# Optimization experiments

Measured on AMD Instinct MI355X. Metric: run time of the kernel, lower is better.

## Reference

```python
import jax, jax.numpy as jnp
import numpy as np

N_NODES = 10000
N_EDGES = 320000
IN_DIM = 512
HID = 64
H0 = 8
OUT = 64
H1 = 1
NEG_SLOPE = 0.2


def gat_layer(h, src, dst, W, attn_l, attn_r, n_nodes, activation=None):
    # h: (N, F_in); W: (F_in, H*D); attn_l/attn_r: (H, D)
    H, D = attn_l.shape
    feat = (h @ W).reshape(n_nodes, H, D)            # (N, H, D)
    el = jnp.einsum('nhd,hd->nh', feat, attn_l)      # (N, H)
    er = jnp.einsum('nhd,hd->nh', feat, attn_r)      # (N, H)
    e = jax.nn.leaky_relu(el[src] + er[dst], NEG_SLOPE)  # (E, H)
    # edge softmax over incoming edges of each destination node
    m = jax.ops.segment_max(e, dst, num_segments=n_nodes)   # (N, H), -inf for isolated
    m = jnp.where(jnp.isfinite(m), m, 0.0)
    ex = jnp.exp(e - m[dst])                         # (E, H)
    s = jax.ops.segment_sum(ex, dst, num_segments=n_nodes)  # (N, H)
    alpha = ex / s[dst]                              # (E, H)
    # weighted aggregation: out[dst] += alpha * feat[src]
    out = jax.ops.segment_sum(alpha[:, :, None] * feat[src], dst,
                              num_segments=n_nodes)  # (N, H, D)
    if activation is not None:
        out = activation(out)
    return out


def setup_inputs() -> dict:
    key = jax.random.key(0)
    ks = jax.random.split(key, 9)
    h = jax.random.normal(ks[0], (N_NODES, IN_DIM), dtype=jnp.float32)
    src = jax.random.randint(ks[1], (N_EDGES,), 0, N_NODES, dtype=jnp.int32)
    dst = jax.random.randint(ks[2], (N_EDGES,), 0, N_NODES, dtype=jnp.int32)
    W1 = jax.random.normal(ks[3], (IN_DIM, H0 * HID), dtype=jnp.float32) / np.sqrt(IN_DIM)
    attn_l1 = jax.random.normal(ks[4], (H0, HID), dtype=jnp.float32) / np.sqrt(HID)
    attn_r1 = jax.random.normal(ks[5], (H0, HID), dtype=jnp.float32) / np.sqrt(HID)
    W2 = jax.random.normal(ks[6], (H0 * HID, H1 * OUT), dtype=jnp.float32) / np.sqrt(H0 * HID)
    attn_l2 = jax.random.normal(ks[7], (H1, OUT), dtype=jnp.float32) / np.sqrt(OUT)
    attn_r2 = jax.random.normal(ks[8], (H1, OUT), dtype=jnp.float32) / np.sqrt(OUT)
    return {"h": h, "src": src, "dst": dst, "W1": W1, "attn_l1": attn_l1,
            "attn_r1": attn_r1, "W2": W2, "attn_l2": attn_l2, "attn_r2": attn_r2}


def reference(h, src, dst, W1, attn_l1, attn_r1, W2, attn_l2, attn_r2):
    # layer 1: elu activation, concat heads (flatten)
    x = gat_layer(h, src, dst, W1, attn_l1, attn_r1, N_NODES, activation=jax.nn.elu)
    x = x.reshape(N_NODES, H0 * HID)
    # layer 2: no activation, mean over heads
    x = gat_layer(x, src, dst, W2, attn_l2, attn_r2, N_NODES, activation=None)
    return x.mean(axis=1)  # (N, OUT)
```

## Files before the change

kernel.cpp:

```cpp
#include <hip/hip_runtime.h>
#include <hip/hip_bf16.h>
#include <math.h>

typedef unsigned int u32;
typedef unsigned short ushort;

constexpr int N_NODES = 10000;
constexpr int N_EDGES = 320000;
constexpr float NEG_SLOPE = 0.2f;

typedef __attribute__((ext_vector_type(8))) _Float16 half8;
typedef __attribute__((ext_vector_type(4))) float f32x4;
typedef __attribute__((ext_vector_type(16))) float f32x16;

__device__ __forceinline__ float lrelu(float x) { return x > 0.f ? x : NEG_SLOPE * x; }
__device__ __forceinline__ float elu(float x)   { return x > 0.f ? x : (expf(x) - 1.f); }

__device__ __forceinline__ ushort f2h(float x) {
    _Float16 h = (_Float16)x;
    return __builtin_bit_cast(ushort, h);
}
__device__ __forceinline__ float h2f(ushort u) {
    return (float)__builtin_bit_cast(_Float16, u);
}

__device__ __forceinline__ void gload16(const void* g, void* l) {
    __builtin_amdgcn_global_load_lds(
        (__attribute__((address_space(1))) void*)g,
        (__attribute__((address_space(3))) void*)l, 16, 0, 0);
}

constexpr int NB_HIST  = (N_EDGES + 255) / 256;
constexpr int NB_T1    = 64;
constexpr int NB_T2    = 8;
constexpr int NB_WLR2  = 2;
constexpr int NB_PRE   = NB_HIST + NB_T1 + NB_T2 + NB_WLR2;
constexpr int NB_SPLIT = (N_NODES * 512 / 4) / 256;

__global__ void prep1_kernel(const float4* __restrict__ h4,
                             ushort* __restrict__ xh,
                             const int* __restrict__ dst, int* __restrict__ counts,
                             int* __restrict__ rank,
                             const float* __restrict__ W1, ushort* __restrict__ w1t,
                             const float* __restrict__ W2, ushort* __restrict__ w2t,
                             const float* __restrict__ al2, const float* __restrict__ ar2,
                             float* __restrict__ wl2, float* __restrict__ wr2) {
    __shared__ float smem[64][65];
    const int b = blockIdx.x;
    if (b < NB_HIST) {
        const int i = b * 256 + threadIdx.x;
        if (i < N_EDGES) rank[i] = atomicAdd(&counts[dst[i]], 1);
    } else if (b < NB_HIST + NB_T1 + NB_T2) {
        const int t0 = b - NB_HIST;
        const bool isW1 = t0 < NB_T1;
        const float* W = isW1 ? W1 : W2;
        ushort* wt = isW1 ? w1t : w2t;
        const int N  = isW1 ? 512 : 64;
        const int t  = isW1 ? t0 : (t0 - NB_T1);
        const int ti = isW1 ? (t & 7) : t;
        const int tj = isW1 ? (t >> 3) : 0;
        const int c  = threadIdx.x & 63;
        const int r0 = threadIdx.x >> 6;
#pragma unroll
        for (int p = 0; p < 16; p++) {
            const int r = p * 4 + r0;
            smem[r][c] = W[(size_t)(ti * 64 + r) * N + tj * 64 + c];
        }
        __syncthreads();
#pragma unroll
        for (int p = 0; p < 16; p++) {
            const int rr = p * 4 + r0;
            wt[(size_t)(tj * 64 + rr) * 512 + ti * 64 + c] = f2h(smem[c][rr]);
        }
    } else if (b < NB_PRE) {
        const int k = (b - NB_HIST - NB_T1 - NB_T2) * 256 + threadIdx.x;
        float sl = 0.f, sr = 0.f;
#pragma unroll 8
        for (int d = 0; d < 64; d++) {
            const float w = W2[(size_t)k * 64 + d];
            sl += w * al2[d];
            sr += w * ar2[d];
        }
        wl2[k] = sl;
        wr2[k] = sr;
    } else {
        const int i = (b - NB_PRE) * 256 + threadIdx.x;
        const float4 v = h4[i];
        *(ushort4*)&xh[i * 4] = make_ushort4(f2h(v.x), f2h(v.y), f2h(v.z), f2h(v.w));
    }
}

__global__ void prep2_scan_kernel(const int* __restrict__ counts, int* __restrict__ offs) {
    __shared__ int wsum[4];
    const int tid = threadIdx.x;
    const int lane = tid & 63, wave = tid >> 6;
    const int base = tid * 40;
    int v[40];
    int s = 0;
#pragma unroll
    for (int i = 0; i < 40; i++) {
        v[i] = (base + i < N_NODES) ? counts[base + i] : 0;
        s += v[i];
    }
    int ps = s;
#pragma unroll
    for (int o = 1; o < 64; o <<= 1) {
        const int t = __shfl_up(ps, o);
        if (lane >= o) ps += t;
    }
    if (lane == 63) wsum[wave] = ps;
    __syncthreads();
    if (tid < 4) {
        int t = wsum[tid];
#pragma unroll
        for (int o = 1; o < 4; o <<= 1) {
            const int u = __shfl_up(t, o);
            if (tid >= o) t += u;
        }
        wsum[tid] = t;
    }
    __syncthreads();
    const int wbase = (wave > 0) ? wsum[wave - 1] : 0;
    int run = wbase + ps - s;
#pragma unroll
    for (int i = 0; i < 40; i++) {
        if (base + i < N_NODES) offs[base + i + 1] = run + v[i];
        run += v[i];
    }
    if (tid == 0) offs[0] = 0;
}

constexpr int NB_GEMM1 = ((N_NODES + 63) / 64) * 4;
constexpr int NB_SCAT  = (N_EDGES + 255) / 256;

__global__ __launch_bounds__(256) void gemm1_scatter_kernel(
    const ushort* __restrict__ A, const ushort* __restrict__ B,
    ushort* __restrict__ Cout, int M,
    const float* __restrict__ attn_l, const float* __restrict__ attn_r,
    float* __restrict__ elp, float* __restrict__ erp,
    const int* __restrict__ src, const int* __restrict__ dst,
    const int* __restrict__ rank, const int* __restrict__ offs,
    int* __restrict__ srcs) {
    constexpr int BM = 64, BN = 128, BK = 64, K = 512, N = 512;

    if ((int)blockIdx.x >= NB_GEMM1) {
        const int i = ((int)blockIdx.x - NB_GEMM1) * 256 + threadIdx.x;
        if (i < N_EDGES) srcs[offs[dst[i]] + rank[i]] = src[i];
        return;
    }

    __shared__ __align__(16) ushort sA[2][BM * BK];
    __shared__ __align__(16) ushort sB[2][BN * BK];

    const int tid = threadIdx.x;
    const int wave = tid >> 6, lane = tid & 63;
    const int m0 = ((int)blockIdx.x >> 2) * BM, n0 = ((int)blockIdx.x & 3) * BN;
    const int wm = wave >> 1, wn = wave & 1;
    const int l31 = lane & 31, lh = lane >> 5;

    size_t abyte[2]; int afb[2];
#pragma unroll
    for (int p = 0; p < 2; p++) {
        const int fb = tid * 16 + p * 4096;
        const int r = fb >> 7, s = (fb >> 4) & 7;
        int ar = m0 + r; if (ar > M - 1) ar = M - 1;
        abyte[p] = (size_t)ar * (K * 2) + (size_t)((s ^ (r & 7)) << 4);
        afb[p] = fb;
    }
    size_t bbyte[4]; int bfb[4];
#pragma unroll
    for (int p = 0; p < 4; p++) {
        const int fb = tid * 16 + p * 4096;
        const int r = fb >> 7, s = (fb >> 4) & 7;
        bbyte[p] = (size_t)(n0 + r) * (K * 2) + (size_t)((s ^ (r & 7)) << 4);
        bfb[p] = fb;
    }

    f32x16 acc[2] = {};

    const int rA = wm * 32 + l31;
    const u32 aoff = rA * 128, axr = rA & 7;
    u32 boff[2], bxr[2];
#pragma unroll
    for (int ni = 0; ni < 2; ni++) {
        const int rB = wn * 64 + ni * 32 + l31;
        boff[ni] = rB * 128; bxr[ni] = rB & 7;
    }

#pragma unroll
    for (int p = 0; p < 2; p++) gload16((const char*)A + abyte[p], (char*)&sA[0][0] + afb[p]);
#pragma unroll
    for (int p = 0; p < 4; p++) gload16((const char*)B + bbyte[p], (char*)&sB[0][0] + bfb[p]);
    __syncthreads();

    int cur = 0;
    for (int k0 = 0; k0 < K; k0 += BK) {
        if (k0 + BK < K) {
            const size_t kb = (size_t)(k0 + BK) * 2;
#pragma unroll
            for (int p = 0; p < 2; p++)
                gload16((const char*)A + abyte[p] + kb, (char*)&sA[cur ^ 1][0] + afb[p]);
#pragma unroll
            for (int p = 0; p < 4; p++)
                gload16((const char*)B + bbyte[p] + kb, (char*)&sB[cur ^ 1][0] + bfb[p]);
        }
        const char* pA = (const char*)&sA[cur][0];
        const char* pB = (const char*)&sB[cur][0];
#pragma unroll
        for (int ks = 0; ks < 4; ks++) {
            const u32 sl = ks * 2 + lh;
            const half8 ah = *(const half8*)(pA + aoff + ((sl ^ axr) << 4));
#pragma unroll
            for (int ni = 0; ni < 2; ni++) {
                const half8 bh = *(const half8*)(pB + boff[ni] + ((sl ^ bxr[ni]) << 4));
                acc[ni] = __builtin_amdgcn_mfma_f32_32x32x16_f16(ah, bh, acc[ni], 0, 0, 0);
            }
        }
        __syncthreads();
        cur ^= 1;
    }

#pragma unroll
    for (int reg = 0; reg < 16; reg++) {
        const int grow = m0 + wm * 32 + (reg & 3) + 8 * (reg >> 2) + 4 * lh;
        if (grow < M) {
#pragma unroll
            for (int ni = 0; ni < 2; ni++) {
                const int gcol = n0 + wn * 64 + ni * 32 + l31;
                Cout[(size_t)grow * N + gcol] = f2h(acc[ni][reg]);
            }
        }
    }

    const int head = (n0 + wn * 64) >> 6;
    float alv[2], arv[2];
#pragma unroll
    for (int ni = 0; ni < 2; ni++) {
        alv[ni] = attn_l[head * 64 + ni * 32 + l31];
        arv[ni] = attn_r[head * 64 + ni * 32 + l31];
    }
#pragma unroll
    for (int reg = 0; reg < 16; reg++) {
        float pl = acc[0][reg] * alv[0] + acc[1][reg] * alv[1];
        float pr = acc[0][reg] * arv[0] + acc[1][reg] * arv[1];
#pragma unroll
        for (int o = 1; o < 32; o <<= 1) {
            pl += __shfl_xor(pl, o);
            pr += __shfl_xor(pr, o);
        }
        const int grow = m0 + wm * 32 + (reg & 3) + 8 * (reg >> 2) + 4 * lh;
        if (l31 == 0 && grow < M) {
            elp[grow * 8 + head] = pl;
            erp[grow * 8 + head] = pr;
        }
    }
}

__global__ __launch_bounds__(256) void gemm2_kernel(
    const ushort* __restrict__ A, const ushort* __restrict__ B,
    ushort* __restrict__ Cout, int M) {
    constexpr int BM = 32, BN = 64, BK = 64, K = 512, N = 64;

    __shared__ __align__(16) ushort sA[2][BM * BK];
    __shared__ __align__(16) ushort sB[2][BN * BK];

    const int tid = threadIdx.x;
    const int wave = tid >> 6, lane = tid & 63;
    const int m0 = blockIdx.x * BM;
    const int wm = wave >> 1, wn = wave & 1;
    const int quad = lane >> 4, l15 = lane & 15;

    const int fa = tid * 16;
    const int ra = fa >> 7, sa_ = (fa >> 4) & 7;
    int arow = m0 + ra; if (arow > M - 1) arow = M - 1;
    const size_t abyte = (size_t)arow * (K * 2) + (size_t)((sa_ ^ (ra & 7)) << 4);

    size_t bbyte[2]; int bfb[2];
#pragma unroll
    for (int p = 0; p < 2; p++) {
        const int fb = tid * 16 + p * 4096;
        const int r = fb >> 7, s = (fb >> 4) & 7;
        bbyte[p] = (size_t)r * (K * 2) + (size_t)((s ^ (r & 7)) << 4);
        bfb[p] = fb;
    }

    f32x4 acc[2] = {};
    const int rA = wm * 16 + l15;
    const u32 aoff = rA * 128, axr = rA & 7;
    u32 boff[2], bxr[2];
#pragma unroll
    for (int ni = 0; ni < 2; ni++) {
        const int rB = wn * 32 + ni * 16 + l15;
        boff[ni] = rB * 128; bxr[ni] = rB & 7;
    }

    gload16((const char*)A + abyte, (char*)&sA[0][0] + fa);
#pragma unroll
    for (int p = 0; p < 2; p++) gload16((const char*)B + bbyte[p], (char*)&sB[0][0] + bfb[p]);
    __syncthreads();

    int cur = 0;
    for (int k0 = 0; k0 < K; k0 += BK) {
        if (k0 + BK < K) {
            const size_t kb = (size_t)(k0 + BK) * 2;
            gload16((const char*)A + abyte + kb, (char*)&sA[cur ^ 1][0] + fa);
#pragma unroll
            for (int p = 0; p < 2; p++)
                gload16((const char*)B + bbyte[p] + kb, (char*)&sB[cur ^ 1][0] + bfb[p]);
        }
        const char* pA = (const char*)&sA[cur][0];
        const char* pB = (const char*)&sB[cur][0];
#pragma unroll
        for (int ks = 0; ks < 2; ks++) {
            const u32 sl = ks * 4 + quad;
            const half8 ah = *(const half8*)(pA + aoff + ((sl ^ axr) << 4));
#pragma unroll
            for (int ni = 0; ni < 2; ni++) {
                const half8 bh = *(const half8*)(pB + boff[ni] + ((sl ^ bxr[ni]) << 4));
                acc[ni] = __builtin_amdgcn_mfma_f32_16x16x32_f16(ah, bh, acc[ni], 0, 0, 0);
            }
        }
        __syncthreads();
        cur ^= 1;
    }

#pragma unroll
    for (int r = 0; r < 4; r++) {
        const int grow = m0 + wm * 16 + quad * 4 + r;
        if (grow < M) {
#pragma unroll
            for (int ni = 0; ni < 2; ni++) {
                const int gcol = wn * 32 + ni * 16 + l15;
                Cout[(size_t)grow * N + gcol] = f2h(acc[ni][r]);
            }
        }
    }
}

__global__ __launch_bounds__(256) void agg1_kernel(
    const ushort* __restrict__ feat, const float* __restrict__ el,
    const float* __restrict__ er, const int* __restrict__ offs,
    const int* __restrict__ srcs, ushort* __restrict__ xh,
    const float* __restrict__ wl2, const float* __restrict__ wr2,
    float* __restrict__ el2, float* __restrict__ er2) {
    const int tid = threadIdx.x;
    const int wave = tid >> 6, lane = tid & 63;
    const int node = blockIdx.x * 4 + wave;
    const int start = offs[node];
    const int deg = offs[node + 1] - start;
    const int d0 = lane * 8;
    const int myh = lane >> 3;

    if (deg == 0) {
        const ushort4 z = make_ushort4(0, 0, 0, 0);
        *(ushort4*)&xh[(size_t)node * 512 + d0] = z;
        *(ushort4*)&xh[(size_t)node * 512 + d0 + 4] = z;
        if (lane == 0) { el2[node] = 0.f; er2[node] = 0.f; }
        return;
    }

    const float4 ea = *(const float4*)&er[node * 8];
    const float4 eb = *(const float4*)&er[node * 8 + 4];
    const float er_my = (myh & 4) ? ((myh & 2) ? ((myh & 1) ? eb.w : eb.z)
                                              : ((myh & 1) ? eb.y : eb.x))
                                  : ((myh & 2) ? ((myh & 1) ? ea.w : ea.z)
                                              : ((myh & 1) ? ea.y : ea.x));

    float acc[8];
#pragma unroll
    for (int i = 0; i < 8; i++) acc[i] = 0.f;
    float ws = 0.f;

    for (int base = 0; base < deg; base += 64) {
        const int has = min(64, deg - base);
        const int s = srcs[start + base + min(lane, has - 1)];
        int j = 0;
        for (; j + 8 <= has; j += 8) {
            int sq[8];
#pragma unroll
            for (int q = 0; q < 8; q++) sq[q] = __shfl(s, j + q);
            float eq[8];
#pragma unroll
            for (int q = 0; q < 8; q++) eq[q] = el[sq[q] * 8 + myh];
            half8 uq[8];
#pragma unroll
            for (int q = 0; q < 8; q++)
                uq[q] = *(const half8*)&feat[(size_t)sq[q] * 512 + d0];
            float wq[8];
#pragma unroll
            for (int q = 0; q < 8; q++) wq[q] = __expf(lrelu(eq[q] + er_my));
#pragma unroll
            for (int q = 0; q < 8; q++) {
#pragma unroll
                for (int i = 0; i < 8; i++)
                    acc[i] += wq[q] * (float)uq[q][i];
                ws += wq[q];
            }
        }
        for (; j < has; j++) {
            const int sj = __shfl(s, j);
            const float w = __expf(lrelu(el[sj * 8 + myh] + er_my));
            const half8 u = *(const half8*)&feat[(size_t)sj * 512 + d0];
#pragma unroll
            for (int i = 0; i < 8; i++)
                acc[i] += w * (float)u[i];
            ws += w;
        }
    }

    const float inv = 1.f / ws;
    float o[8];
#pragma unroll
    for (int i = 0; i < 8; i++) o[i] = elu(acc[i] * inv);

    const float4 wla = *(const float4*)&wl2[d0];
    const float4 wlb = *(const float4*)&wl2[d0 + 4];
    const float4 wra = *(const float4*)&wr2[d0];
    const float4 wrb = *(const float4*)&wr2[d0 + 4];
    float pl = o[0] * wla.x + o[1] * wla.y + o[2] * wla.z + o[3] * wla.w
             + o[4] * wlb.x + o[5] * wlb.y + o[6] * wlb.z + o[7] * wlb.w;
    float pr = o[0] * wra.x + o[1] * wra.y + o[2] * wra.z + o[3] * wra.w
             + o[4] * wrb.x + o[5] * wrb.y + o[6] * wrb.z + o[7] * wrb.w;
#pragma unroll
    for (int off = 32; off > 0; off >>= 1) {
        pl += __shfl_xor(pl, off);
        pr += __shfl_xor(pr, off);
    }
    if (lane == 0) { el2[node] = pl; er2[node] = pr; }

    ushort hh[8];
#pragma unroll
    for (int i = 0; i < 8; i++) hh[i] = f2h(o[i]);
    *(ushort4*)&xh[(size_t)node * 512 + d0]     = make_ushort4(hh[0], hh[1], hh[2], hh[3]);
    *(ushort4*)&xh[(size_t)node * 512 + d0 + 4] = make_ushort4(hh[4], hh[5], hh[6], hh[7]);
}

__global__ __launch_bounds__(256) void agg2_kernel(
    const ushort* __restrict__ feat, const float* __restrict__ el,
    const float* __restrict__ er, const int* __restrict__ offs,
    const int* __restrict__ srcs, float* __restrict__ out) {
    const int tid = threadIdx.x;
    const int wave = tid >> 6, lane = tid & 63;
    const int node = blockIdx.x * 4 + wave;
    const int start = offs[node];
    const int deg = offs[node + 1] - start;
    if (deg == 0) { out[(size_t)node * 64 + lane] = 0.f; return; }
    const float ern = er[node];

    float acc = 0.f, ws = 0.f;
    for (int base = 0; base < deg; base += 64) {
        const int has = min(64, deg - base);
        const int s = srcs[start + base + min(lane, has - 1)];
        const float w = __expf(lrelu(el[s] + ern));
        int j = 0;
        for (; j + 8 <= has; j += 8) {
            float aq[8]; int sq[8];
#pragma unroll
            for (int q = 0; q < 8; q++) { aq[q] = __shfl(w, j + q); sq[q] = __shfl(s, j + q); }
            ushort fq[8];
#pragma unroll
            for (int q = 0; q < 8; q++) fq[q] = feat[(size_t)sq[q] * 64 + lane];
#pragma unroll
            for (int q = 0; q < 8; q++) { acc += aq[q] * h2f(fq[q]); ws += aq[q]; }
        }
        for (; j < has; j++) {
            const float a = __shfl(w, j);
            const int sj = __shfl(s, j);
            acc += a * h2f(feat[(size_t)sj * 64 + lane]);
            ws += a;
        }
    }
    out[(size_t)node * 64 + lane] = acc / ws;
}

extern "C" void kernel_launch(void* const* d_in, const int* in_sizes, int n_in,
                              void* d_out, int out_size, void* d_ws, size_t ws_size,
                              hipStream_t stream) {
    const float* h   = (const float*)d_in[0];
    const int*   src = (const int*)d_in[1];
    const int*   dst = (const int*)d_in[2];
    const float* W1  = (const float*)d_in[3];
    const float* al1 = (const float*)d_in[4];
    const float* ar1 = (const float*)d_in[5];
    const float* W2  = (const float*)d_in[6];
    const float* al2 = (const float*)d_in[7];
    const float* ar2 = (const float*)d_in[8];
    float* out = (float*)d_out;

    char* p = (char*)d_ws;
    ushort* feat1 = (ushort*)p; p += (size_t)N_NODES * 512 * 2;
    ushort* feat2 = (ushort*)p; p += (size_t)N_NODES * 64 * 2;
    float* el1   = (float*)p;  p += (size_t)N_NODES * 8 * 4;
    float* er1   = (float*)p;  p += (size_t)N_NODES * 8 * 4;
    float* el2   = (float*)p;  p += (size_t)N_NODES * 4;
    float* er2   = (float*)p;  p += (size_t)N_NODES * 4;
    ushort* xh   = (ushort*)p; p += (size_t)N_NODES * 512 * 2;
    ushort* w1t  = (ushort*)p; p += (size_t)512 * 512 * 2;
    ushort* w2t  = (ushort*)p; p += (size_t)64 * 512 * 2;
    float* wl2   = (float*)p;  p += (size_t)512 * 4;
    float* wr2   = (float*)p;  p += (size_t)512 * 4;
    int* counts  = (int*)p;    p += (size_t)N_NODES * 4;
    int* offs    = (int*)p;    p += (size_t)10004 * 4;
    int* rank    = (int*)p;    p += (size_t)N_EDGES * 4;
    int* srcs    = (int*)p;    p += (size_t)N_EDGES * 4;

    hipMemsetAsync(counts, 0, (size_t)N_NODES * 4, stream);

    prep1_kernel<<<NB_PRE + NB_SPLIT, 256, 0, stream>>>(
        (const float4*)h, xh, dst, counts, rank,
        W1, w1t, W2, w2t, al2, ar2, wl2, wr2);

    prep2_scan_kernel<<<1, 256, 0, stream>>>(counts, offs);

    gemm1_scatter_kernel<<<NB_GEMM1 + NB_SCAT, 256, 0, stream>>>(
        xh, w1t, feat1, N_NODES, al1, ar1, el1, er1,
        src, dst, rank, offs, srcs);

    agg1_kernel<<<N_NODES / 4, 256, 0, stream>>>(
        feat1, el1, er1, offs, srcs, xh, wl2, wr2, el2, er2);

    gemm2_kernel<<<(N_NODES + 31) / 32, 256, 0, stream>>>(
        xh, w2t, feat2, N_NODES);

    agg2_kernel<<<N_NODES / 4, 256, 0, stream>>>(feat2, el2, er2, offs, srcs, out);
}
```

Baseline: 194.4 us.

## Replace global atomic degree histogram with per-chunk LDS histograms and chunk scan

The destination-degree histogram now uses 64 chunked blocks. Each block counts its edges with LDS atomics into a full 10000-entry shared array and writes per-chunk counts to global memory. A new kernel scans these counts across chunks per node, and the scatter step adds the chunk offset. This removes contended global atomics and the memset, at the cost of an extra kernel launch, a 2.5 MB count buffer, 40 KB of LDS on every prep1 block (which lowers occupancy for the other branches), and only 64 blocks doing the histogram work.

```diff
diff --git a/kernel.cpp b/kernel.cpp
--- a/kernel.cpp
+++ b/kernel.cpp
@@ -30,28 +30,40 @@
         (__attribute__((address_space(3))) void*)l, 16, 0, 0);
 }
 
-constexpr int NB_HIST  = (N_EDGES + 255) / 256;
+constexpr int NCHUNK = 64;
+constexpr int EPC    = N_EDGES / NCHUNK;
 constexpr int NB_T1    = 64;
 constexpr int NB_T2    = 8;
 constexpr int NB_WLR2  = 2;
-constexpr int NB_PRE   = NB_HIST + NB_T1 + NB_T2 + NB_WLR2;
+constexpr int NB_PRE   = NCHUNK + NB_T1 + NB_T2 + NB_WLR2;
 constexpr int NB_SPLIT = (N_NODES * 512 / 4) / 256;
 
-__global__ void prep1_kernel(const float4* __restrict__ h4,
+__global__ __launch_bounds__(256) void prep1_kernel(
+                             const float4* __restrict__ h4,
                              ushort* __restrict__ xh,
-                             const int* __restrict__ dst, int* __restrict__ counts,
+                             const int* __restrict__ dst, int* __restrict__ ccnt,
                              int* __restrict__ rank,
                              const float* __restrict__ W1, ushort* __restrict__ w1t,
                              const float* __restrict__ W2, ushort* __restrict__ w2t,
                              const float* __restrict__ al2, const float* __restrict__ ar2,
                              float* __restrict__ wl2, float* __restrict__ wr2) {
-    __shared__ float smem[64][65];
+    __shared__ __align__(16) int shbuf[N_NODES];
     const int b = blockIdx.x;
-    if (b < NB_HIST) {
-        const int i = b * 256 + threadIdx.x;
-        if (i < N_EDGES) rank[i] = atomicAdd(&counts[dst[i]], 1);
-    } else if (b < NB_HIST + NB_T1 + NB_T2) {
-        const int t0 = b - NB_HIST;
+    if (b < NCHUNK) {
+        for (int i = threadIdx.x; i < N_NODES; i += 256) shbuf[i] = 0;
+        __syncthreads();
+        const int e0 = b * EPC;
+#pragma unroll 4
+        for (int i = threadIdx.x; i < EPC; i += 256) {
+            const int e = e0 + i;
+            rank[e] = atomicAdd(&shbuf[dst[e]], 1);
+        }
+        __syncthreads();
+        for (int i = threadIdx.x; i < N_NODES; i += 256)
+            ccnt[b * N_NODES + i] = shbuf[i];
+    } else if (b < NCHUNK + NB_T1 + NB_T2) {
+        float* smem = (float*)shbuf;
+        const int t0 = b - NCHUNK;
         const bool isW1 = t0 < NB_T1;
         const float* W = isW1 ? W1 : W2;
         ushort* wt = isW1 ? w1t : w2t;
@@ -64,16 +76,16 @@
 #pragma unroll
         for (int p = 0; p < 16; p++) {
             const int r = p * 4 + r0;
-            smem[r][c] = W[(size_t)(ti * 64 + r) * N + tj * 64 + c];
+            smem[r * 65 + c] = W[(size_t)(ti * 64 + r) * N + tj * 64 + c];
         }
         __syncthreads();
 #pragma unroll
         for (int p = 0; p < 16; p++) {
             const int rr = p * 4 + r0;
-            wt[(size_t)(tj * 64 + rr) * 512 + ti * 64 + c] = f2h(smem[c][rr]);
+            wt[(size_t)(tj * 64 + rr) * 512 + ti * 64 + c] = f2h(smem[c * 65 + rr]);
         }
     } else if (b < NB_PRE) {
-        const int k = (b - NB_HIST - NB_T1 - NB_T2) * 256 + threadIdx.x;
+        const int k = (b - NCHUNK - NB_T1 - NB_T2) * 256 + threadIdx.x;
         float sl = 0.f, sr = 0.f;
 #pragma unroll 8
         for (int d = 0; d < 64; d++) {
@@ -88,6 +100,23 @@
         const float4 v = h4[i];
         *(ushort4*)&xh[i * 4] = make_ushort4(f2h(v.x), f2h(v.y), f2h(v.z), f2h(v.w));
     }
+}
+
+__global__ __launch_bounds__(256) void chunkscan_kernel(int* __restrict__ ccnt,
+                                                        int* __restrict__ counts) {
+    const int n = blockIdx.x * 256 + threadIdx.x;
+    if (n >= N_NODES) return;
+    int v[NCHUNK];
+#pragma unroll
+    for (int c = 0; c < NCHUNK; c++) v[c] = ccnt[c * N_NODES + n];
+    int run = 0;
+#pragma unroll
+    for (int c = 0; c < NCHUNK; c++) {
+        const int t = v[c];
+        ccnt[c * N_NODES + n] = run;
+        run += t;
+    }
+    counts[n] = run;
 }
 
 __global__ void prep2_scan_kernel(const int* __restrict__ counts, int* __restrict__ offs) {
@@ -140,12 +169,16 @@
     float* __restrict__ elp, float* __restrict__ erp,
     const int* __restrict__ src, const int* __restrict__ dst,
     const int* __restrict__ rank, const int* __restrict__ offs,
-    int* __restrict__ srcs) {
+    const int* __restrict__ ccnt, int* __restrict__ srcs) {
     constexpr int BM = 64, BN = 128, BK = 64, K = 512, N = 512;
 
     if ((int)blockIdx.x >= NB_GEMM1) {
         const int i = ((int)blockIdx.x - NB_GEMM1) * 256 + threadIdx.x;
-        if (i < N_EDGES) srcs[offs[dst[i]] + rank[i]] = src[i];
+        if (i < N_EDGES) {
+            const int c = i / EPC;
+            const int d = dst[i];
+            srcs[offs[d] + ccnt[c * N_NODES + d] + rank[i]] = src[i];
+        }
         return;
     }
 
@@ -500,21 +533,22 @@
     float* wl2   = (float*)p;  p += (size_t)512 * 4;
     float* wr2   = (float*)p;  p += (size_t)512 * 4;
     int* counts  = (int*)p;    p += (size_t)N_NODES * 4;
+    int* ccnt    = (int*)p;    p += (size_t)NCHUNK * N_NODES * 4;
     int* offs    = (int*)p;    p += (size_t)10004 * 4;
     int* rank    = (int*)p;    p += (size_t)N_EDGES * 4;
     int* srcs    = (int*)p;    p += (size_t)N_EDGES * 4;
 
-    hipMemsetAsync(counts, 0, (size_t)N_NODES * 4, stream);
-
     prep1_kernel<<<NB_PRE + NB_SPLIT, 256, 0, stream>>>(
-        (const float4*)h, xh, dst, counts, rank,
+        (const float4*)h, xh, dst, ccnt, rank,
         W1, w1t, W2, w2t, al2, ar2, wl2, wr2);
+
+    chunkscan_kernel<<<(N_NODES + 255) / 256, 256, 0, stream>>>(ccnt, counts);
 
     prep2_scan_kernel<<<1, 256, 0, stream>>>(counts, offs);
 
     gemm1_scatter_kernel<<<NB_GEMM1 + NB_SCAT, 256, 0, stream>>>(
         xh, w1t, feat1, N_NODES, al1, ar1, el1, er1,
-        src, dst, rank, offs, srcs);
+        src, dst, rank, offs, ccnt, srcs);
 
     agg1_kernel<<<N_NODES / 4, 256, 0, stream>>>(
         feat1, el1, er1, offs, srcs, xh, wl2, wr2, el2, er2);
```

New measurement: 182.1 us. -6.3%, faster.
